# Kernel optimization log

Hardware: AMD Instinct MI355X
Metric: run time of the kernel (lower is better)

## Reference

```python
import math
import jax, jax.numpy as jnp
import numpy as np


def setup_inputs() -> dict:
    key = jax.random.key(0)
    k1, k2 = jax.random.split(key)
    N, H, W, h, d = 32, 32, 32, 16, 64
    input_NHWhd = jax.random.normal(k1, (N, H, W, h, d), dtype=jnp.float32)
    emb_2dd = jax.random.uniform(k2, (2, d, d), dtype=jnp.float32) * (2.0 * math.pi)
    return {"input_NHWhd": input_NHWhd, "emb_2dd": emb_2dd}


def _positions(H, W):
    # xlim = sqrt(W/H), ylim = sqrt(H/W); positions stacked as (y, x)
    xlim = math.sqrt(W / H)
    ylim = math.sqrt(H / W)
    x_HW = jnp.broadcast_to(jnp.linspace(-xlim, xlim, W, dtype=jnp.float32)[None, :], (H, W))
    y_HW = jnp.broadcast_to(jnp.linspace(-ylim, ylim, H, dtype=jnp.float32)[:, None], (H, W))
    return jnp.stack((y_HW, x_HW), axis=-1)  # [H, W, 2]


def reference(input_NHWhd, emb_2dd):
    N, H, W, h, d = input_NHWhd.shape
    # skew-symmetric generator bases (the -0.5 shift cancels in M - M^T,
    # kept for faithfulness to the original)
    upper_2dd = jnp.triu(emb_2dd, k=1) - 0.5
    skew_2dd = upper_2dd - jnp.swapaxes(upper_2dd, -2, -1)  # [2, d, d]
    pos_HW2 = _positions(H, W)
    # per-position generator: sum over the 2 spatial components
    gen_HWdd = jnp.einsum("hwc,cij->hwij", pos_HW2, skew_2dd)  # [H, W, d, d]
    rot_HWdd = jax.vmap(jax.scipy.linalg.expm)(gen_HWdd.reshape(-1, d, d)).reshape(H, W, d, d)
    # apply rotation: out[n,y,x,q,:] = input[n,y,x,q,:] @ rot[y,x]
    out_NHWhd = jnp.einsum("nhwqd,hwde->nhwqe", input_NHWhd, rot_HWdd.astype(input_NHWhd.dtype))
    return out_NHWhd
```

## Files before the change

### kernel.cpp

```cpp
#include <hip/hip_runtime.h>


typedef float f4 __attribute__((ext_vector_type(4)));
typedef short s8v __attribute__((ext_vector_type(8)));
typedef float f32x4 __attribute__((ext_vector_type(4)));
typedef unsigned short ush;
typedef unsigned int u32;
typedef ush us4 __attribute__((ext_vector_type(4)));

constexpr int LST = 68;
constexpr int BST = 72;
constexpr int SLOT = 64 * BST;

static __device__ __forceinline__ ush f2bf(float f) {
    u32 u = __float_as_uint(f);
    u += 0x7fffu + ((u >> 16) & 1u);
    return (ush)(u >> 16);
}
static __device__ __forceinline__ float bf2f(ush h) {
    return __uint_as_float(((u32)h) << 16);
}
static __device__ __forceinline__ s8v negbf(s8v v) {
    u32* p = (u32*)&v;
#pragma unroll
    for (int i = 0; i < 4; ++i) p[i] ^= 0x80008000u;
    return v;
}

static __device__ __forceinline__ void load_frag(
    s8v fr[2][2][2], const ush* __restrict__ ah, const ush* __restrict__ al,
    int m, int q4, int base, bool neg)
{
#pragma unroll
    for (int t = 0; t < 2; ++t)
#pragma unroll
        for (int ks = 0; ks < 2; ++ks) {
            const int off = (base + t * 16 + m) * BST + ks * 32 + q4 * 8;
            s8v h = *(const s8v*)&ah[off];
            s8v l = *(const s8v*)&al[off];
            if (neg) { h = negbf(h); l = negbf(l); }
            fr[t][ks][0] = h;
            fr[t][ks][1] = l;
        }
}

static __device__ __forceinline__ void mm_pre(
    ush* __restrict__ dh, ush* __restrict__ dl,
    const s8v pa[2][2][2],
    const ush* __restrict__ qh, const ush* __restrict__ ql,
    float cdiag, int m, int q4, int DM, int DN)
{
    s8v qb[2][2][2];
    load_frag(qb, qh, ql, m, q4, DN, false);

    f32x4 acc[2][2];
#pragma unroll
    for (int mt = 0; mt < 2; ++mt)
#pragma unroll
        for (int nt = 0; nt < 2; ++nt) acc[mt][nt] = (f32x4){0.f, 0.f, 0.f, 0.f};

#pragma unroll
    for (int ks = 0; ks < 2; ++ks)
#pragma unroll
        for (int mt = 0; mt < 2; ++mt)
#pragma unroll
            for (int nt = 0; nt < 2; ++nt) {
                acc[mt][nt] = __builtin_amdgcn_mfma_f32_16x16x32_bf16(
                    pa[mt][ks][0], qb[nt][ks][0], acc[mt][nt], 0, 0, 0);
                acc[mt][nt] = __builtin_amdgcn_mfma_f32_16x16x32_bf16(
                    pa[mt][ks][0], qb[nt][ks][1], acc[mt][nt], 0, 0, 0);
                acc[mt][nt] = __builtin_amdgcn_mfma_f32_16x16x32_bf16(
                    pa[mt][ks][1], qb[nt][ks][0], acc[mt][nt], 0, 0, 0);
            }

#pragma unroll
    for (int mt = 0; mt < 2; ++mt)
#pragma unroll
        for (int nt = 0; nt < 2; ++nt) {
            const int gm = DM + mt * 16 + q4 * 4;
            const int gn = DN + nt * 16 + m;
            us4 h4, l4;
#pragma unroll
            for (int r = 0; r < 4; ++r) {
                float v = acc[mt][nt][r];
                if (gn == gm + r) v += cdiag;
                const ush h = f2bf(v);
                h4[r] = h;
                l4[r] = f2bf(v - bf2f(h));
            }
            *(us4*)&dh[gn * BST + gm] = h4;
            *(us4*)&dl[gn * BST + gm] = l4;
        }
}

static __device__ __forceinline__ void transp(
    ush* __restrict__ dh, ush* __restrict__ dl,
    const ush* __restrict__ sh, const ush* __restrict__ sl, int tid)
{
    const int r = tid & 63;
    const int k0 = (tid >> 6) << 4;
    s8v a0 = *(const s8v*)&sh[r * BST + k0];
    s8v a1 = *(const s8v*)&sh[r * BST + k0 + 8];
    s8v b0 = *(const s8v*)&sl[r * BST + k0];
    s8v b1 = *(const s8v*)&sl[r * BST + k0 + 8];
#pragma unroll
    for (int j = 0; j < 8; ++j) {
        dh[(k0 + j) * BST + r]     = ((const ush*)&a0)[j];
        dh[(k0 + j + 8) * BST + r] = ((const ush*)&a1)[j];
        dl[(k0 + j) * BST + r]     = ((const ush*)&b0)[j];
        dl[(k0 + j + 8) * BST + r] = ((const ush*)&b1)[j];
    }
}

__global__ __launch_bounds__(256, 2)
void liere_fused(const float* __restrict__ in, const float* __restrict__ emb,
                 float* __restrict__ out) {
    __shared__ __align__(16) ush buf[6 * SLOT];
    __shared__ float snorm;

    const int tid = threadIdx.x;
    const int p = blockIdx.x;
    const int y = p >> 5;
    const int x = p & 31;

    float* sG = (float*)(buf);
    float* sU = (float*)(buf + 2 * SLOT);
    float* sV = (float*)(buf + 4 * SLOT);

#pragma unroll
    for (int i = 0; i < 4; ++i) {
        int lin = i * 1024 + tid * 4;
        int r = lin >> 6, c = lin & 63;
        *(f4*)&sU[r * LST + c] = *(const f4*)&emb[lin];
        *(f4*)&sV[r * LST + c] = *(const f4*)&emb[4096 + lin];
    }
    __syncthreads();

    const float yv = (2.0f * (float)y - 31.0f) / 31.0f;
    const float xv = (2.0f * (float)x - 31.0f) / 31.0f;
    {
        const int r0 = (tid >> 4) << 2, c0 = (tid & 15) << 2;
#pragma unroll
        for (int i = 0; i < 4; ++i)
#pragma unroll
            for (int j = 0; j < 4; ++j) {
                int r = r0 + i, c = c0 + j;
                float s0, s1;
                if (r < c)      { s0 = sU[r * LST + c];  s1 = sV[r * LST + c]; }
                else if (r > c) { s0 = -sU[c * LST + r]; s1 = -sV[c * LST + r]; }
                else            { s0 = 0.f; s1 = 0.f; }
                sG[r * LST + c] = yv * s0 + xv * s1;
            }
    }
    __syncthreads();

    if (tid < 64) {
        float s = 0.f;
        for (int c = 0; c < 64; ++c) s += fabsf(sG[tid * LST + c]);
#pragma unroll
        for (int off = 32; off > 0; off >>= 1) s = fmaxf(s, __shfl_down(s, off, 64));
        if (tid == 0) snorm = s;
    }
    __syncthreads();
    int sq = 0;
    {
        float nm = snorm;
        if (nm > 1.0f) sq = (int)ceilf(log2f(nm));
        if (sq < 0) sq = 0;
        if (sq > 14) sq = 14;
    }
    const float scale = exp2f((float)(-sq));

    const float C9 = 2.75573192e-6f, C8 = 2.48015876e-5f, C7 = 1.98412701e-4f,
                C6 = 1.38888893e-3f, C5 = 8.33333377e-3f, C4 = 4.16666679e-2f,
                C3 = 0.166666672f,   C2 = 0.5f,           C1 = 1.0f, C0 = 1.0f;

    ush* Xh = buf + 2 * SLOT;  ush* Xl = buf + 3 * SLOT;
    ush* t_h = buf + 4 * SLOT; ush* t_l = buf + 5 * SLOT;
    ush* u_h = buf + 0 * SLOT; ush* u_l = buf + 1 * SLOT;

    {
        const int r0 = (tid >> 4) << 2, c0 = (tid & 15) << 2;
#pragma unroll
        for (int i = 0; i < 4; ++i)
#pragma unroll
            for (int j = 0; j < 4; ++j) {
                int r = r0 + i, c = c0 + j;
                float a = sG[r * LST + c] * scale;
                ush xh = f2bf(a);
                Xh[r * BST + c] = xh;
                Xl[r * BST + c] = f2bf(a - bf2f(xh));
                float t0 = C9 * a + ((r == c) ? C8 : 0.f);
                ush th = f2bf(t0);
                t_h[r * BST + c] = th;
                t_l[r * BST + c] = f2bf(t0 - bf2f(th));
            }
    }
    __syncthreads();

    const int lane = tid & 63;
    const int w = tid >> 6;
    const int m = lane & 15;
    const int q4 = lane >> 4;
    const int DM = (w & 1) * 32;
    const int DN = (w >> 1) * 32;

    s8v xf[2][2][2];
    load_frag(xf, Xh, Xl, m, q4, DM, true);

    const float cs[8] = {C7, C6, C5, C4, C3, C2, C1, C0};
#pragma unroll
    for (int s = 0; s < 8; ++s) {
        mm_pre(u_h, u_l, xf, t_h, t_l, cs[s], m, q4, DM, DN);
        __syncthreads();
        ush* th2 = t_h; t_h = u_h; u_h = th2;
        ush* tl2 = t_l; t_l = u_l; u_l = tl2;
    }
    ush* tt_h = Xh; ush* tt_l = Xl;
    transp(tt_h, tt_l, t_h, t_l, tid);
    __syncthreads();

    for (int i = 0; i < sq; ++i) {
        s8v af[2][2][2];
        load_frag(af, tt_h, tt_l, m, q4, DM, false);
        mm_pre(u_h, u_l, af, t_h, t_l, 0.f, m, q4, DM, DN);
        __syncthreads();
        transp(tt_h, tt_l, u_h, u_l, tid);
        __syncthreads();
        ush* th2 = t_h; t_h = u_h; u_h = th2;
        ush* tl2 = t_l; t_l = u_l; u_l = tl2;
    }

    const int pass = w >> 1;
    const int nbase = (w & 1) << 4;

    const ush* RF = pass ? t_h : tt_h;
    s8v rf[4][2];
#pragma unroll
    for (int t = 0; t < 4; ++t) {
        rf[t][0] = *(const s8v*)&RF[(t * 16 + m) * BST + q4 * 8];
        rf[t][1] = *(const s8v*)&RF[(t * 16 + m) * BST + 32 + q4 * 8];
    }

    const int yy = pass ? (31 - y) : y;
    const int xx = pass ? (31 - x) : x;
    const size_t pos = (size_t)(yy * 32 + xx) * 1024;

    for (int i = 0; i < 16; ++i) {
        const int n = nbase + i;
        const size_t nb = (size_t)n << 20;
        const float* src = in + nb + pos + m * 64 + q4 * 8;
        f4 u0 = *(const f4*)src;
        f4 u1 = *(const f4*)(src + 4);
        f4 u2 = *(const f4*)(src + 32);
        f4 u3 = *(const f4*)(src + 36);
        s8v b0, b1;
        b0[0] = (short)f2bf(u0.x); b0[1] = (short)f2bf(u0.y);
        b0[2] = (short)f2bf(u0.z); b0[3] = (short)f2bf(u0.w);
        b0[4] = (short)f2bf(u1.x); b0[5] = (short)f2bf(u1.y);
        b0[6] = (short)f2bf(u1.z); b0[7] = (short)f2bf(u1.w);
        b1[0] = (short)f2bf(u2.x); b1[1] = (short)f2bf(u2.y);
        b1[2] = (short)f2bf(u2.z); b1[3] = (short)f2bf(u2.w);
        b1[4] = (short)f2bf(u3.x); b1[5] = (short)f2bf(u3.y);
        b1[6] = (short)f2bf(u3.z); b1[7] = (short)f2bf(u3.w);

        f32x4 acc0 = {0.f,0.f,0.f,0.f}, acc1 = acc0, acc2 = acc0, acc3 = acc0;
        acc0 = __builtin_amdgcn_mfma_f32_16x16x32_bf16(rf[0][0], b0, acc0, 0, 0, 0);
        acc0 = __builtin_amdgcn_mfma_f32_16x16x32_bf16(rf[0][1], b1, acc0, 0, 0, 0);
        acc1 = __builtin_amdgcn_mfma_f32_16x16x32_bf16(rf[1][0], b0, acc1, 0, 0, 0);
        acc1 = __builtin_amdgcn_mfma_f32_16x16x32_bf16(rf[1][1], b1, acc1, 0, 0, 0);
        acc2 = __builtin_amdgcn_mfma_f32_16x16x32_bf16(rf[2][0], b0, acc2, 0, 0, 0);
        acc2 = __builtin_amdgcn_mfma_f32_16x16x32_bf16(rf[2][1], b1, acc2, 0, 0, 0);
        acc3 = __builtin_amdgcn_mfma_f32_16x16x32_bf16(rf[3][0], b0, acc3, 0, 0, 0);
        acc3 = __builtin_amdgcn_mfma_f32_16x16x32_bf16(rf[3][1], b1, acc3, 0, 0, 0);

        float* dst = out + nb + pos + m * 64 + q4 * 4;
        f4 o0 = {acc0[0], acc0[1], acc0[2], acc0[3]};
        f4 o1 = {acc1[0], acc1[1], acc1[2], acc1[3]};
        f4 o2 = {acc2[0], acc2[1], acc2[2], acc2[3]};
        f4 o3 = {acc3[0], acc3[1], acc3[2], acc3[3]};
        *(f4*)(dst +  0) = o0;
        *(f4*)(dst + 16) = o1;
        *(f4*)(dst + 32) = o2;
        *(f4*)(dst + 48) = o3;
    }
}

extern "C" void kernel_launch(void* const* d_in, const int* in_sizes, int n_in,
                              void* d_out, int out_size, void* d_ws, size_t ws_size,
                              hipStream_t stream) {
    (void)in_sizes; (void)n_in; (void)out_size; (void)d_ws; (void)ws_size;
    const float* in = (const float*)d_in[0];
    const float* emb = (const float*)d_in[1];
    float* out = (float*)d_out;
    hipLaunchKernelGGL(liere_fused, dim3(512), dim3(256), 0, stream, in, emb, out);
}
```

Measured before the change: 263.6 us.

## Split fused kernel into expm precompute and high-occupancy apply kernels

Splits the single fused kernel in two. The first kernel computes the rotation matrices (expm via Taylor series plus squaring) and writes them as bf16 to workspace. The second applies them with 2048 blocks at a higher occupancy bound, so the memory-bound apply phase gets more parallelism. It also replaces the manual bf16 rounding with the packed v_cvt_pk_bf16_f32 instruction. The cost is an extra launch plus a workspace round trip, and the old fused path is kept as a fallback when no workspace is available.

After: 287.2 us. 9.0% more time.

```diff
diff --git a/kernel.cpp b/kernel.cpp
--- a/kernel.cpp
+++ b/kernel.cpp
@@ -25,6 +25,11 @@
 #pragma unroll
     for (int i = 0; i < 4; ++i) p[i] ^= 0x80008000u;
     return v;
+}
+static __device__ __forceinline__ u32 cvtpk(float a, float b) {
+    u32 r;
+    asm("v_cvt_pk_bf16_f32 %0, %1, %2" : "=v"(r) : "v"(a), "v"(b));
+    return r;
 }
 
 static __device__ __forceinline__ void load_frag(
@@ -113,8 +118,7 @@
 }
 
 __global__ __launch_bounds__(256, 2)
-void liere_fused(const float* __restrict__ in, const float* __restrict__ emb,
-                 float* __restrict__ out) {
+void liere_expm(const float* __restrict__ emb, ush* __restrict__ ws) {
     __shared__ __align__(16) ush buf[6 * SLOT];
     __shared__ float snorm;
 
@@ -230,49 +234,71 @@
         ush* th2 = t_h; t_h = u_h; u_h = th2;
         ush* tl2 = t_l; t_l = u_l; u_l = tl2;
     }
-
-    const int pass = w >> 1;
-    const int nbase = (w & 1) << 4;
-
-    const ush* RF = pass ? t_h : tt_h;
+    {
+        const int pos0 = y * 32 + x;
+        const int pos1 = (31 - y) * 32 + (31 - x);
+        ush* A0 = ws + (size_t)pos0 * 4096;
+        ush* A1 = ws + (size_t)pos1 * 4096;
+        const int r = tid >> 2;
+        const int c = (tid & 3) << 4;
+        s8v v0 = *(const s8v*)&tt_h[r * BST + c];
+        s8v v1 = *(const s8v*)&tt_h[r * BST + c + 8];
+        s8v w0 = *(const s8v*)&t_h[r * BST + c];
+        s8v w1 = *(const s8v*)&t_h[r * BST + c + 8];
+        *(s8v*)&A0[r * 64 + c] = v0;
+        *(s8v*)&A0[r * 64 + c + 8] = v1;
+        *(s8v*)&A1[r * 64 + c] = w0;
+        *(s8v*)&A1[r * 64 + c + 8] = w1;
+    }
+}
+
+__global__ __launch_bounds__(256, 5)
+void liere_apply(const float* __restrict__ in, const ush* __restrict__ ws,
+                 float* __restrict__ out) {
+    const int tid = threadIdx.x;
+    const int b = blockIdx.x;
+    const int posid = b >> 1;
+    const int half = b & 1;
+    const int w = tid >> 6;
+    const int lane = tid & 63;
+    const int m = lane & 15;
+    const int q4 = lane >> 4;
+
+    const ush* RF = ws + (size_t)posid * 4096;
     s8v rf[4][2];
 #pragma unroll
     for (int t = 0; t < 4; ++t) {
-        rf[t][0] = *(const s8v*)&RF[(t * 16 + m) * BST + q4 * 8];
-        rf[t][1] = *(const s8v*)&RF[(t * 16 + m) * BST + 32 + q4 * 8];
-    }
-
-    const int yy = pass ? (31 - y) : y;
-    const int xx = pass ? (31 - x) : x;
-    const size_t pos = (size_t)(yy * 32 + xx) * 1024;
-
-    for (int i = 0; i < 16; ++i) {
-        const int n = nbase + i;
+        rf[t][0] = *(const s8v*)&RF[(t * 16 + m) * 64 + q4 * 8];
+        rf[t][1] = *(const s8v*)&RF[(t * 16 + m) * 64 + 32 + q4 * 8];
+    }
+
+    const size_t pos = (size_t)posid * 1024;
+    const int n0 = half * 16 + w * 4;
+
+    for (int i = 0; i < 4; ++i) {
+        const int n = n0 + i;
         const size_t nb = (size_t)n << 20;
         const float* src = in + nb + pos + m * 64 + q4 * 8;
         f4 u0 = *(const f4*)src;
         f4 u1 = *(const f4*)(src + 4);
         f4 u2 = *(const f4*)(src + 32);
         f4 u3 = *(const f4*)(src + 36);
-        s8v b0, b1;
-        b0[0] = (short)f2bf(u0.x); b0[1] = (short)f2bf(u0.y);
-        b0[2] = (short)f2bf(u0.z); b0[3] = (short)f2bf(u0.w);
-        b0[4] = (short)f2bf(u1.x); b0[5] = (short)f2bf(u1.y);
-        b0[6] = (short)f2bf(u1.z); b0[7] = (short)f2bf(u1.w);
-        b1[0] = (short)f2bf(u2.x); b1[1] = (short)f2bf(u2.y);
-        b1[2] = (short)f2bf(u2.z); b1[3] = (short)f2bf(u2.w);
-        b1[4] = (short)f2bf(u3.x); b1[5] = (short)f2bf(u3.y);
-        b1[6] = (short)f2bf(u3.z); b1[7] = (short)f2bf(u3.w);
+
+        union { s8v v; u32 wv[4]; } B0, B1;
+        B0.wv[0] = cvtpk(u0.x, u0.y); B0.wv[1] = cvtpk(u0.z, u0.w);
+        B0.wv[2] = cvtpk(u1.x, u1.y); B0.wv[3] = cvtpk(u1.z, u1.w);
+        B1.wv[0] = cvtpk(u2.x, u2.y); B1.wv[1] = cvtpk(u2.z, u2.w);
+        B1.wv[2] = cvtpk(u3.x, u3.y); B1.wv[3] = cvtpk(u3.z, u3.w);
 
         f32x4 acc0 = {0.f,0.f,0.f,0.f}, acc1 = acc0, acc2 = acc0, acc3 = acc0;
-        acc0 = __builtin_amdgcn_mfma_f32_16x16x32_bf16(rf[0][0], b0, acc0, 0, 0, 0);
-        acc0 = __builtin_amdgcn_mfma_f32_16x16x32_bf16(rf[0][1], b1, acc0, 0, 0, 0);
-        acc1 = __builtin_amdgcn_mfma_f32_16x16x32_bf16(rf[1][0], b0, acc1, 0, 0, 0);
-        acc1 = __builtin_amdgcn_mfma_f32_16x16x32_bf16(rf[1][1], b1, acc1, 0, 0, 0);
-        acc2 = __builtin_amdgcn_mfma_f32_16x16x32_bf16(rf[2][0], b0, acc2, 0, 0, 0);
-        acc2 = __builtin_amdgcn_mfma_f32_16x16x32_bf16(rf[2][1], b1, acc2, 0, 0, 0);
-        acc3 = __builtin_amdgcn_mfma_f32_16x16x32_bf16(rf[3][0], b0, acc3, 0, 0, 0);
-        acc3 = __builtin_amdgcn_mfma_f32_16x16x32_bf16(rf[3][1], b1, acc3, 0, 0, 0);
+        acc0 = __builtin_amdgcn_mfma_f32_16x16x32_bf16(rf[0][0], B0.v, acc0, 0, 0, 0);
+        acc0 = __builtin_amdgcn_mfma_f32_16x16x32_bf16(rf[0][1], B1.v, acc0, 0, 0, 0);
+        acc1 = __builtin_amdgcn_mfma_f32_16x16x32_bf16(rf[1][0], B0.v, acc1, 0, 0, 0);
+        acc1 = __builtin_amdgcn_mfma_f32_16x16x32_bf16(rf[1][1], B1.v, acc1, 0, 0, 0);
+        acc2 = __builtin_amdgcn_mfma_f32_16x16x32_bf16(rf[2][0], B0.v, acc2, 0, 0, 0);
+        acc2 = __builtin_amdgcn_mfma_f32_16x16x32_bf16(rf[2][1], B1.v, acc2, 0, 0, 0);
+        acc3 = __builtin_amdgcn_mfma_f32_16x16x32_bf16(rf[3][0], B0.v, acc3, 0, 0, 0);
+        acc3 = __builtin_amdgcn_mfma_f32_16x16x32_bf16(rf[3][1], B1.v, acc3, 0, 0, 0);
 
         float* dst = out + nb + pos + m * 64 + q4 * 4;
         f4 o0 = {acc0[0], acc0[1], acc0[2], acc0[3]};
@@ -286,12 +312,189 @@
     }
 }
 
+__global__ __launch_bounds__(256, 2)
+void liere_fused(const float* __restrict__ in, const float* __restrict__ emb,
+                 float* __restrict__ out) {
+    __shared__ __align__(16) ush buf[6 * SLOT];
+    __shared__ float snorm;
+
+    const int tid = threadIdx.x;
+    const int p = blockIdx.x;
+    const int y = p >> 5;
+    const int x = p & 31;
+
+    float* sG = (float*)(buf);
+    float* sU = (float*)(buf + 2 * SLOT);
+    float* sV = (float*)(buf + 4 * SLOT);
+
+#pragma unroll
+    for (int i = 0; i < 4; ++i) {
+        int lin = i * 1024 + tid * 4;
+        int r = lin >> 6, c = lin & 63;
+        *(f4*)&sU[r * LST + c] = *(const f4*)&emb[lin];
+        *(f4*)&sV[r * LST + c] = *(const f4*)&emb[4096 + lin];
+    }
+    __syncthreads();
+
+    const float yv = (2.0f * (float)y - 31.0f) / 31.0f;
+    const float xv = (2.0f * (float)x - 31.0f) / 31.0f;
+    {
+        const int r0 = (tid >> 4) << 2, c0 = (tid & 15) << 2;
+#pragma unroll
+        for (int i = 0; i < 4; ++i)
+#pragma unroll
+            for (int j = 0; j < 4; ++j) {
+                int r = r0 + i, c = c0 + j;
+                float s0, s1;
+                if (r < c)      { s0 = sU[r * LST + c];  s1 = sV[r * LST + c]; }
+                else if (r > c) { s0 = -sU[c * LST + r]; s1 = -sV[c * LST + r]; }
+                else            { s0 = 0.f; s1 = 0.f; }
+                sG[r * LST + c] = yv * s0 + xv * s1;
+            }
+    }
+    __syncthreads();
+
+    if (tid < 64) {
+        float s = 0.f;
+        for (int c = 0; c < 64; ++c) s += fabsf(sG[tid * LST + c]);
+#pragma unroll
+        for (int off = 32; off > 0; off >>= 1) s = fmaxf(s, __shfl_down(s, off, 64));
+        if (tid == 0) snorm = s;
+    }
+    __syncthreads();
+    int sq = 0;
+    {
+        float nm = snorm;
+        if (nm > 1.0f) sq = (int)ceilf(log2f(nm));
+        if (sq < 0) sq = 0;
+        if (sq > 14) sq = 14;
+    }
+    const float scale = exp2f((float)(-sq));
+
+    const float C9 = 2.75573192e-6f, C8 = 2.48015876e-5f, C7 = 1.98412701e-4f,
+                C6 = 1.38888893e-3f, C5 = 8.33333377e-3f, C4 = 4.16666679e-2f,
+                C3 = 0.166666672f,   C2 = 0.5f,           C1 = 1.0f, C0 = 1.0f;
+
+    ush* Xh = buf + 2 * SLOT;  ush* Xl = buf + 3 * SLOT;
+    ush* t_h = buf + 4 * SLOT; ush* t_l = buf + 5 * SLOT;
+    ush* u_h = buf + 0 * SLOT; ush* u_l = buf + 1 * SLOT;
+
+    {
+        const int r0 = (tid >> 4) << 2, c0 = (tid & 15) << 2;
+#pragma unroll
+        for (int i = 0; i < 4; ++i)
+#pragma unroll
+            for (int j = 0; j < 4; ++j) {
+                int r = r0 + i, c = c0 + j;
+                float a = sG[r * LST + c] * scale;
+                ush xh = f2bf(a);
+                Xh[r * BST + c] = xh;
+                Xl[r * BST + c] = f2bf(a - bf2f(xh));
+                float t0 = C9 * a + ((r == c) ? C8 : 0.f);
+                ush th = f2bf(t0);
+                t_h[r * BST + c] = th;
+                t_l[r * BST + c] = f2bf(t0 - bf2f(th));
+            }
+    }
+    __syncthreads();
+
+    const int lane = tid & 63;
+    const int w = tid >> 6;
+    const int m = lane & 15;
+    const int q4 = lane >> 4;
+    const int DM = (w & 1) * 32;
+    const int DN = (w >> 1) * 32;
+
+    s8v xf[2][2][2];
+    load_frag(xf, Xh, Xl, m, q4, DM, true);
+
+    const float cs[8] = {C7, C6, C5, C4, C3, C2, C1, C0};
+#pragma unroll
+    for (int s = 0; s < 8; ++s) {
+        mm_pre(u_h, u_l, xf, t_h, t_l, cs[s], m, q4, DM, DN);
+        __syncthreads();
+        ush* th2 = t_h; t_h = u_h; u_h = th2;
+        ush* tl2 = t_l; t_l = u_l; u_l = tl2;
+    }
+    ush* tt_h = Xh; ush* tt_l = Xl;
+    transp(tt_h, tt_l, t_h, t_l, tid);
+    __syncthreads();
+
+    for (int i = 0; i < sq; ++i) {
+        s8v af[2][2][2];
+        load_frag(af, tt_h, tt_l, m, q4, DM, false);
+        mm_pre(u_h, u_l, af, t_h, t_l, 0.f, m, q4, DM, DN);
+        __syncthreads();
+        transp(tt_h, tt_l, u_h, u_l, tid);
+        __syncthreads();
+        ush* th2 = t_h; t_h = u_h; u_h = th2;
+        ush* tl2 = t_l; t_l = u_l; u_l = tl2;
+    }
+
+    const int pass = w >> 1;
+    const int nbase = (w & 1) << 4;
+
+    const ush* RF = pass ? t_h : tt_h;
+    s8v rf[4][2];
+#pragma unroll
+    for (int t = 0; t < 4; ++t) {
+        rf[t][0] = *(const s8v*)&RF[(t * 16 + m) * BST + q4 * 8];
+        rf[t][1] = *(const s8v*)&RF[(t * 16 + m) * BST + 32 + q4 * 8];
+    }
+
+    const int yy = pass ? (31 - y) : y;
+    const int xx = pass ? (31 - x) : x;
+    const size_t pos = (size_t)(yy * 32 + xx) * 1024;
+
+    for (int i = 0; i < 16; ++i) {
+        const int n = nbase + i;
+        const size_t nb = (size_t)n << 20;
+        const float* src = in + nb + pos + m * 64 + q4 * 8;
+        f4 u0 = *(const f4*)src;
+        f4 u1 = *(const f4*)(src + 4);
+        f4 u2 = *(const f4*)(src + 32);
+        f4 u3 = *(const f4*)(src + 36);
+        union { s8v v; u32 wv[4]; } B0, B1;
+        B0.wv[0] = cvtpk(u0.x, u0.y); B0.wv[1] = cvtpk(u0.z, u0.w);
+        B0.wv[2] = cvtpk(u1.x, u1.y); B0.wv[3] = cvtpk(u1.z, u1.w);
+        B1.wv[0] = cvtpk(u2.x, u2.y); B1.wv[1] = cvtpk(u2.z, u2.w);
+        B1.wv[2] = cvtpk(u3.x, u3.y); B1.wv[3] = cvtpk(u3.z, u3.w);
+
+        f32x4 acc0 = {0.f,0.f,0.f,0.f}, acc1 = acc0, acc2 = acc0, acc3 = acc0;
+        acc0 = __builtin_amdgcn_mfma_f32_16x16x32_bf16(rf[0][0], B0.v, acc0, 0, 0, 0);
+        acc0 = __builtin_amdgcn_mfma_f32_16x16x32_bf16(rf[0][1], B1.v, acc0, 0, 0, 0);
+        acc1 = __builtin_amdgcn_mfma_f32_16x16x32_bf16(rf[1][0], B0.v, acc1, 0, 0, 0);
+        acc1 = __builtin_amdgcn_mfma_f32_16x16x32_bf16(rf[1][1], B1.v, acc1, 0, 0, 0);
+        acc2 = __builtin_amdgcn_mfma_f32_16x16x32_bf16(rf[2][0], B0.v, acc2, 0, 0, 0);
+        acc2 = __builtin_amdgcn_mfma_f32_16x16x32_bf16(rf[2][1], B1.v, acc2, 0, 0, 0);
+        acc3 = __builtin_amdgcn_mfma_f32_16x16x32_bf16(rf[3][0], B0.v, acc3, 0, 0, 0);
+        acc3 = __builtin_amdgcn_mfma_f32_16x16x32_bf16(rf[3][1], B1.v, acc3, 0, 0, 0);
+
+        float* dst = out + nb + pos + m * 64 + q4 * 4;
+        f4 o0 = {acc0[0], acc0[1], acc0[2], acc0[3]};
+        f4 o1 = {acc1[0], acc1[1], acc1[2], acc1[3]};
+        f4 o2 = {acc2[0], acc2[1], acc2[2], acc2[3]};
+        f4 o3 = {acc3[0], acc3[1], acc3[2], acc3[3]};
+        *(f4*)(dst +  0) = o0;
+        *(f4*)(dst + 16) = o1;
+        *(f4*)(dst + 32) = o2;
+        *(f4*)(dst + 48) = o3;
+    }
+}
+
 extern "C" void kernel_launch(void* const* d_in, const int* in_sizes, int n_in,
                               void* d_out, int out_size, void* d_ws, size_t ws_size,
                               hipStream_t stream) {
-    (void)in_sizes; (void)n_in; (void)out_size; (void)d_ws; (void)ws_size;
+    (void)in_sizes; (void)n_in; (void)out_size;
     const float* in = (const float*)d_in[0];
     const float* emb = (const float*)d_in[1];
     float* out = (float*)d_out;
-    hipLaunchKernelGGL(liere_fused, dim3(512), dim3(256), 0, stream, in, emb, out);
-}
+    const size_t need = (size_t)1024 * 4096 * sizeof(ush);
+    if (d_ws != nullptr && ws_size >= need) {
+        ush* ws = (ush*)d_ws;
+        hipLaunchKernelGGL(liere_expm, dim3(512), dim3(256), 0, stream, emb, ws);
+        hipLaunchKernelGGL(liere_apply, dim3(2048), dim3(256), 0, stream, in, ws, out);
+    } else {
+        hipLaunchKernelGGL(liere_fused, dim3(512), dim3(256), 0, stream, in, emb, out);
+    }
+}
```

## Use 512-thread blocks with in-place matmul chains and packed bf16 conversion

Applied to the files above, without the earlier changes.

Doubles the block size to 512 threads and splits the 64x64 matrix work so each wave computes a 32x16 tile. Shared memory drops from six slots to four by writing the Horner and squaring results in place, separated by extra barriers. The row-norm reduction now uses shuffles instead of a serial shared-memory loop, and the squaring loop writes the transposed copy directly instead of running a separate transpose pass. Input conversion uses the packed v_cvt_pk_bf16_f32 instruction. Each block still handles two mirrored positions, with more waves streaming the batch dimension, at the cost of more barriers per step.

Result: slower. 269.4 us (+2.2%).

```diff
diff --git a/kernel.cpp b/kernel.cpp
--- a/kernel.cpp
+++ b/kernel.cpp
@@ -26,8 +26,13 @@
     for (int i = 0; i < 4; ++i) p[i] ^= 0x80008000u;
     return v;
 }
-
-static __device__ __forceinline__ void load_frag(
+static __device__ __forceinline__ u32 cvtpk(float a, float b) {
+    u32 r;
+    asm("v_cvt_pk_bf16_f32 %0, %1, %2" : "=v"(r) : "v"(a), "v"(b));
+    return r;
+}
+
+static __device__ __forceinline__ void load2(
     s8v fr[2][2][2], const ush* __restrict__ ah, const ush* __restrict__ al,
     int m, int q4, int base, bool neg)
 {
@@ -44,158 +49,117 @@
         }
 }
 
-static __device__ __forceinline__ void mm_pre(
-    ush* __restrict__ dh, ush* __restrict__ dl,
-    const s8v pa[2][2][2],
-    const ush* __restrict__ qh, const ush* __restrict__ ql,
-    float cdiag, int m, int q4, int DM, int DN)
+static __device__ __forceinline__ void load1(
+    s8v fr[2][2], const ush* __restrict__ ah, const ush* __restrict__ al,
+    int m, int q4, int base)
 {
-    s8v qb[2][2][2];
-    load_frag(qb, qh, ql, m, q4, DN, false);
-
-    f32x4 acc[2][2];
-#pragma unroll
-    for (int mt = 0; mt < 2; ++mt)
-#pragma unroll
-        for (int nt = 0; nt < 2; ++nt) acc[mt][nt] = (f32x4){0.f, 0.f, 0.f, 0.f};
-
+#pragma unroll
+    for (int ks = 0; ks < 2; ++ks) {
+        const int off = (base + m) * BST + ks * 32 + q4 * 8;
+        fr[ks][0] = *(const s8v*)&ah[off];
+        fr[ks][1] = *(const s8v*)&al[off];
+    }
+}
+
+static __device__ __forceinline__ void mm_core(
+    f32x4 acc[2], const s8v pa[2][2][2], const s8v qb[2][2])
+{
 #pragma unroll
     for (int ks = 0; ks < 2; ++ks)
 #pragma unroll
-        for (int mt = 0; mt < 2; ++mt)
-#pragma unroll
-            for (int nt = 0; nt < 2; ++nt) {
-                acc[mt][nt] = __builtin_amdgcn_mfma_f32_16x16x32_bf16(
-                    pa[mt][ks][0], qb[nt][ks][0], acc[mt][nt], 0, 0, 0);
-                acc[mt][nt] = __builtin_amdgcn_mfma_f32_16x16x32_bf16(
-                    pa[mt][ks][0], qb[nt][ks][1], acc[mt][nt], 0, 0, 0);
-                acc[mt][nt] = __builtin_amdgcn_mfma_f32_16x16x32_bf16(
-                    pa[mt][ks][1], qb[nt][ks][0], acc[mt][nt], 0, 0, 0);
-            }
-
-#pragma unroll
-    for (int mt = 0; mt < 2; ++mt)
-#pragma unroll
-        for (int nt = 0; nt < 2; ++nt) {
-            const int gm = DM + mt * 16 + q4 * 4;
-            const int gn = DN + nt * 16 + m;
-            us4 h4, l4;
-#pragma unroll
-            for (int r = 0; r < 4; ++r) {
-                float v = acc[mt][nt][r];
-                if (gn == gm + r) v += cdiag;
-                const ush h = f2bf(v);
-                h4[r] = h;
-                l4[r] = f2bf(v - bf2f(h));
-            }
-            *(us4*)&dh[gn * BST + gm] = h4;
-            *(us4*)&dl[gn * BST + gm] = l4;
-        }
-}
-
-static __device__ __forceinline__ void transp(
-    ush* __restrict__ dh, ush* __restrict__ dl,
-    const ush* __restrict__ sh, const ush* __restrict__ sl, int tid)
-{
-    const int r = tid & 63;
-    const int k0 = (tid >> 6) << 4;
-    s8v a0 = *(const s8v*)&sh[r * BST + k0];
-    s8v a1 = *(const s8v*)&sh[r * BST + k0 + 8];
-    s8v b0 = *(const s8v*)&sl[r * BST + k0];
-    s8v b1 = *(const s8v*)&sl[r * BST + k0 + 8];
-#pragma unroll
-    for (int j = 0; j < 8; ++j) {
-        dh[(k0 + j) * BST + r]     = ((const ush*)&a0)[j];
-        dh[(k0 + j + 8) * BST + r] = ((const ush*)&a1)[j];
-        dl[(k0 + j) * BST + r]     = ((const ush*)&b0)[j];
-        dl[(k0 + j + 8) * BST + r] = ((const ush*)&b1)[j];
-    }
-}
-
-__global__ __launch_bounds__(256, 2)
-void liere_fused(const float* __restrict__ in, const float* __restrict__ emb,
-                 float* __restrict__ out) {
-    __shared__ __align__(16) ush buf[6 * SLOT];
-    __shared__ float snorm;
+        for (int mt = 0; mt < 2; ++mt) {
+            acc[mt] = __builtin_amdgcn_mfma_f32_16x16x32_bf16(
+                pa[mt][ks][0], qb[ks][0], acc[mt], 0, 0, 0);
+            acc[mt] = __builtin_amdgcn_mfma_f32_16x16x32_bf16(
+                pa[mt][ks][0], qb[ks][1], acc[mt], 0, 0, 0);
+            acc[mt] = __builtin_amdgcn_mfma_f32_16x16x32_bf16(
+                pa[mt][ks][1], qb[ks][0], acc[mt], 0, 0, 0);
+        }
+}
+
+__global__ __launch_bounds__(512, 4)
+void liere_fused2(const float* __restrict__ in, const float* __restrict__ emb,
+                  float* __restrict__ out) {
+    __shared__ __align__(16) ush buf[4 * SLOT];
+    __shared__ float sRed[16];
 
     const int tid = threadIdx.x;
     const int p = blockIdx.x;
     const int y = p >> 5;
     const int x = p & 31;
 
-    float* sG = (float*)(buf);
-    float* sU = (float*)(buf + 2 * SLOT);
-    float* sV = (float*)(buf + 4 * SLOT);
-
-#pragma unroll
-    for (int i = 0; i < 4; ++i) {
-        int lin = i * 1024 + tid * 4;
+    ush* H_A = buf;              ush* L_A = buf + SLOT;
+    ush* H_B = buf + 2 * SLOT;   ush* L_B = buf + 3 * SLOT;
+    float* sE0 = (float*)buf;
+    float* sE1 = (float*)(buf + 2 * SLOT);
+
+#pragma unroll
+    for (int i = 0; i < 2; ++i) {
+        int lin = i * 2048 + tid * 4;
         int r = lin >> 6, c = lin & 63;
-        *(f4*)&sU[r * LST + c] = *(const f4*)&emb[lin];
-        *(f4*)&sV[r * LST + c] = *(const f4*)&emb[4096 + lin];
+        *(f4*)&sE0[r * LST + c] = *(const f4*)&emb[lin];
+        *(f4*)&sE1[r * LST + c] = *(const f4*)&emb[4096 + lin];
     }
     __syncthreads();
 
     const float yv = (2.0f * (float)y - 31.0f) / 31.0f;
     const float xv = (2.0f * (float)x - 31.0f) / 31.0f;
+    const int gr0 = (tid >> 5) << 2;
+    const int gc0 = (tid & 31) << 1;
+    float g[4][2];
+    float rs[4];
+#pragma unroll
+    for (int i = 0; i < 4; ++i) {
+        rs[i] = 0.f;
+#pragma unroll
+        for (int j = 0; j < 2; ++j) {
+            int r = gr0 + i, c = gc0 + j;
+            float s0, s1;
+            if (r < c)      { s0 = sE0[r * LST + c];  s1 = sE1[r * LST + c]; }
+            else if (r > c) { s0 = -sE0[c * LST + r]; s1 = -sE1[c * LST + r]; }
+            else            { s0 = 0.f; s1 = 0.f; }
+            float v = yv * s0 + xv * s1;
+            g[i][j] = v;
+            rs[i] += fabsf(v);
+        }
+    }
+#pragma unroll
+    for (int off = 16; off > 0; off >>= 1) {
+#pragma unroll
+        for (int i = 0; i < 4; ++i) rs[i] += __shfl_xor(rs[i], off, 32);
+    }
     {
-        const int r0 = (tid >> 4) << 2, c0 = (tid & 15) << 2;
-#pragma unroll
-        for (int i = 0; i < 4; ++i)
-#pragma unroll
-            for (int j = 0; j < 4; ++j) {
-                int r = r0 + i, c = c0 + j;
-                float s0, s1;
-                if (r < c)      { s0 = sU[r * LST + c];  s1 = sV[r * LST + c]; }
-                else if (r > c) { s0 = -sU[c * LST + r]; s1 = -sV[c * LST + r]; }
-                else            { s0 = 0.f; s1 = 0.f; }
-                sG[r * LST + c] = yv * s0 + xv * s1;
-            }
+        float mx = fmaxf(fmaxf(rs[0], rs[1]), fmaxf(rs[2], rs[3]));
+        if ((tid & 31) == 0) sRed[tid >> 5] = mx;
     }
     __syncthreads();
-
-    if (tid < 64) {
-        float s = 0.f;
-        for (int c = 0; c < 64; ++c) s += fabsf(sG[tid * LST + c]);
-#pragma unroll
-        for (int off = 32; off > 0; off >>= 1) s = fmaxf(s, __shfl_down(s, off, 64));
-        if (tid == 0) snorm = s;
-    }
-    __syncthreads();
+    float nm = sRed[0];
+#pragma unroll
+    for (int k = 1; k < 16; ++k) nm = fmaxf(nm, sRed[k]);
     int sq = 0;
-    {
-        float nm = snorm;
-        if (nm > 1.0f) sq = (int)ceilf(log2f(nm));
-        if (sq < 0) sq = 0;
-        if (sq > 14) sq = 14;
-    }
+    if (nm > 1.0f) sq = (int)ceilf(log2f(nm));
+    if (sq < 0) sq = 0;
+    if (sq > 14) sq = 14;
     const float scale = exp2f((float)(-sq));
 
     const float C9 = 2.75573192e-6f, C8 = 2.48015876e-5f, C7 = 1.98412701e-4f,
                 C6 = 1.38888893e-3f, C5 = 8.33333377e-3f, C4 = 4.16666679e-2f,
                 C3 = 0.166666672f,   C2 = 0.5f,           C1 = 1.0f, C0 = 1.0f;
 
-    ush* Xh = buf + 2 * SLOT;  ush* Xl = buf + 3 * SLOT;
-    ush* t_h = buf + 4 * SLOT; ush* t_l = buf + 5 * SLOT;
-    ush* u_h = buf + 0 * SLOT; ush* u_l = buf + 1 * SLOT;
-
-    {
-        const int r0 = (tid >> 4) << 2, c0 = (tid & 15) << 2;
-#pragma unroll
-        for (int i = 0; i < 4; ++i)
-#pragma unroll
-            for (int j = 0; j < 4; ++j) {
-                int r = r0 + i, c = c0 + j;
-                float a = sG[r * LST + c] * scale;
-                ush xh = f2bf(a);
-                Xh[r * BST + c] = xh;
-                Xl[r * BST + c] = f2bf(a - bf2f(xh));
-                float t0 = C9 * a + ((r == c) ? C8 : 0.f);
-                ush th = f2bf(t0);
-                t_h[r * BST + c] = th;
-                t_l[r * BST + c] = f2bf(t0 - bf2f(th));
-            }
-    }
+#pragma unroll
+    for (int i = 0; i < 4; ++i)
+#pragma unroll
+        for (int j = 0; j < 2; ++j) {
+            int r = gr0 + i, c = gc0 + j;
+            float a = g[i][j] * scale;
+            ush xh = f2bf(a);
+            H_B[r * BST + c] = xh;
+            L_B[r * BST + c] = f2bf(a - bf2f(xh));
+            float t0 = C9 * a + ((r == c) ? C8 : 0.f);
+            ush th = f2bf(t0);
+            H_A[r * BST + c] = th;
+            L_A[r * BST + c] = f2bf(t0 - bf2f(th));
+        }
     __syncthreads();
 
     const int lane = tid & 63;
@@ -203,38 +167,89 @@
     const int m = lane & 15;
     const int q4 = lane >> 4;
     const int DM = (w & 1) * 32;
-    const int DN = (w >> 1) * 32;
+    const int DN = (w >> 1) * 16;
 
     s8v xf[2][2][2];
-    load_frag(xf, Xh, Xl, m, q4, DM, true);
+    load2(xf, H_B, L_B, m, q4, DM, true);
 
     const float cs[8] = {C7, C6, C5, C4, C3, C2, C1, C0};
-#pragma unroll
     for (int s = 0; s < 8; ++s) {
-        mm_pre(u_h, u_l, xf, t_h, t_l, cs[s], m, q4, DM, DN);
+        s8v qb[2][2];
+        load1(qb, H_A, L_A, m, q4, DN);
         __syncthreads();
-        ush* th2 = t_h; t_h = u_h; u_h = th2;
-        ush* tl2 = t_l; t_l = u_l; u_l = tl2;
-    }
-    ush* tt_h = Xh; ush* tt_l = Xl;
-    transp(tt_h, tt_l, t_h, t_l, tid);
+        f32x4 acc[2];
+        acc[0] = (f32x4){0.f, 0.f, 0.f, 0.f};
+        acc[1] = acc[0];
+        mm_core(acc, xf, qb);
+#pragma unroll
+        for (int mt = 0; mt < 2; ++mt) {
+            const int gm = DM + mt * 16 + q4 * 4;
+            const int gn = DN + m;
+            us4 h4, l4;
+#pragma unroll
+            for (int r = 0; r < 4; ++r) {
+                float v = acc[mt][r];
+                if (gn == gm + r) v += cs[s];
+                const ush h = f2bf(v);
+                h4[r] = h;
+                l4[r] = f2bf(v - bf2f(h));
+            }
+            *(us4*)&H_A[gn * BST + gm] = h4;
+            *(us4*)&L_A[gn * BST + gm] = l4;
+        }
+        __syncthreads();
+    }
+
+    {
+        const int r = tid & 63;
+        const int k0 = (tid >> 6) << 3;
+        s8v a0 = *(const s8v*)&H_A[r * BST + k0];
+        s8v b0 = *(const s8v*)&L_A[r * BST + k0];
+#pragma unroll
+        for (int j = 0; j < 8; ++j) {
+            H_B[(k0 + j) * BST + r] = ((const ush*)&a0)[j];
+            L_B[(k0 + j) * BST + r] = ((const ush*)&b0)[j];
+        }
+    }
     __syncthreads();
 
-    for (int i = 0; i < sq; ++i) {
+    for (int it = 0; it < sq; ++it) {
         s8v af[2][2][2];
-        load_frag(af, tt_h, tt_l, m, q4, DM, false);
-        mm_pre(u_h, u_l, af, t_h, t_l, 0.f, m, q4, DM, DN);
+        load2(af, H_B, L_B, m, q4, DM, false);
+        s8v qb[2][2];
+        load1(qb, H_A, L_A, m, q4, DN);
         __syncthreads();
-        transp(tt_h, tt_l, u_h, u_l, tid);
+        f32x4 acc[2];
+        acc[0] = (f32x4){0.f, 0.f, 0.f, 0.f};
+        acc[1] = acc[0];
+        mm_core(acc, af, qb);
+#pragma unroll
+        for (int mt = 0; mt < 2; ++mt) {
+            const int gm = DM + mt * 16 + q4 * 4;
+            const int gn = DN + m;
+            us4 h4, l4;
+#pragma unroll
+            for (int r = 0; r < 4; ++r) {
+                float v = acc[mt][r];
+                const ush h = f2bf(v);
+                h4[r] = h;
+                l4[r] = f2bf(v - bf2f(h));
+            }
+            *(us4*)&H_A[gn * BST + gm] = h4;
+            *(us4*)&L_A[gn * BST + gm] = l4;
+#pragma unroll
+            for (int r = 0; r < 4; ++r) {
+                H_B[(gm + r) * BST + gn] = h4[r];
+                L_B[(gm + r) * BST + gn] = l4[r];
+            }
+        }
         __syncthreads();
-        ush* th2 = t_h; t_h = u_h; u_h = th2;
-        ush* tl2 = t_l; t_l = u_l; u_l = tl2;
-    }
-
-    const int pass = w >> 1;
-    const int nbase = (w & 1) << 4;
-
-    const ush* RF = pass ? t_h : tt_h;
+    }
+
+    const int pass = w >> 2;
+    const int n0 = (w & 3) * 8;
+
+    const ush* RF = pass ? H_A : H_B;
     s8v rf[4][2];
 #pragma unroll
     for (int t = 0; t < 4; ++t) {
@@ -246,33 +261,30 @@
     const int xx = pass ? (31 - x) : x;
     const size_t pos = (size_t)(yy * 32 + xx) * 1024;
 
-    for (int i = 0; i < 16; ++i) {
-        const int n = nbase + i;
+    for (int i = 0; i < 8; ++i) {
+        const int n = n0 + i;
         const size_t nb = (size_t)n << 20;
         const float* src = in + nb + pos + m * 64 + q4 * 8;
         f4 u0 = *(const f4*)src;
         f4 u1 = *(const f4*)(src + 4);
         f4 u2 = *(const f4*)(src + 32);
         f4 u3 = *(const f4*)(src + 36);
-        s8v b0, b1;
-        b0[0] = (short)f2bf(u0.x); b0[1] = (short)f2bf(u0.y);
-        b0[2] = (short)f2bf(u0.z); b0[3] = (short)f2bf(u0.w);
-        b0[4] = (short)f2bf(u1.x); b0[5] = (short)f2bf(u1.y);
-        b0[6] = (short)f2bf(u1.z); b0[7] = (short)f2bf(u1.w);
-        b1[0] = (short)f2bf(u2.x); b1[1] = (short)f2bf(u2.y);
-        b1[2] = (short)f2bf(u2.z); b1[3] = (short)f2bf(u2.w);
-        b1[4] = (short)f2bf(u3.x); b1[5] = (short)f2bf(u3.y);
-        b1[6] = (short)f2bf(u3.z); b1[7] = (short)f2bf(u3.w);
+
+        union { s8v v; u32 wv[4]; } B0, B1;
+        B0.wv[0] = cvtpk(u0.x, u0.y); B0.wv[1] = cvtpk(u0.z, u0.w);
+        B0.wv[2] = cvtpk(u1.x, u1.y); B0.wv[3] = cvtpk(u1.z, u1.w);
+        B1.wv[0] = cvtpk(u2.x, u2.y); B1.wv[1] = cvtpk(u2.z, u2.w);
+        B1.wv[2] = cvtpk(u3.x, u3.y); B1.wv[3] = cvtpk(u3.z, u3.w);
 
         f32x4 acc0 = {0.f,0.f,0.f,0.f}, acc1 = acc0, acc2 = acc0, acc3 = acc0;
-        acc0 = __builtin_amdgcn_mfma_f32_16x16x32_bf16(rf[0][0], b0, acc0, 0, 0, 0);
-        acc0 = __builtin_amdgcn_mfma_f32_16x16x32_bf16(rf[0][1], b1, acc0, 0, 0, 0);
-        acc1 = __builtin_amdgcn_mfma_f32_16x16x32_bf16(rf[1][0], b0, acc1, 0, 0, 0);
-        acc1 = __builtin_amdgcn_mfma_f32_16x16x32_bf16(rf[1][1], b1, acc1, 0, 0, 0);
-        acc2 = __builtin_amdgcn_mfma_f32_16x16x32_bf16(rf[2][0], b0, acc2, 0, 0, 0);
-        acc2 = __builtin_amdgcn_mfma_f32_16x16x32_bf16(rf[2][1], b1, acc2, 0, 0, 0);
-        acc3 = __builtin_amdgcn_mfma_f32_16x16x32_bf16(rf[3][0], b0, acc3, 0, 0, 0);
-        acc3 = __builtin_amdgcn_mfma_f32_16x16x32_bf16(rf[3][1], b1, acc3, 0, 0, 0);
+        acc0 = __builtin_amdgcn_mfma_f32_16x16x32_bf16(rf[0][0], B0.v, acc0, 0, 0, 0);
+        acc0 = __builtin_amdgcn_mfma_f32_16x16x32_bf16(rf[0][1], B1.v, acc0, 0, 0, 0);
+        acc1 = __builtin_amdgcn_mfma_f32_16x16x32_bf16(rf[1][0], B0.v, acc1, 0, 0, 0);
+        acc1 = __builtin_amdgcn_mfma_f32_16x16x32_bf16(rf[1][1], B1.v, acc1, 0, 0, 0);
+        acc2 = __builtin_amdgcn_mfma_f32_16x16x32_bf16(rf[2][0], B0.v, acc2, 0, 0, 0);
+        acc2 = __builtin_amdgcn_mfma_f32_16x16x32_bf16(rf[2][1], B1.v, acc2, 0, 0, 0);
+        acc3 = __builtin_amdgcn_mfma_f32_16x16x32_bf16(rf[3][0], B0.v, acc3, 0, 0, 0);
+        acc3 = __builtin_amdgcn_mfma_f32_16x16x32_bf16(rf[3][1], B1.v, acc3, 0, 0, 0);
 
         float* dst = out + nb + pos + m * 64 + q4 * 4;
         f4 o0 = {acc0[0], acc0[1], acc0[2], acc0[3]};
@@ -293,5 +305,5 @@
     const float* in = (const float*)d_in[0];
     const float* emb = (const float*)d_in[1];
     float* out = (float*)d_out;
-    hipLaunchKernelGGL(liere_fused, dim3(512), dim3(256), 0, stream, in, emb, out);
-}
+    hipLaunchKernelGGL(liere_fused2, dim3(512), dim3(512), 0, stream, in, emb, out);
+}
```
